# Kernel optimization log

Hardware: AMD Instinct MI355X
Metric: run time of the kernel (lower is better)

The kernel has to match this reference:

```python
import jax, jax.numpy as jnp
import numpy as np

B, S, D, H = 2, 2048, 1024, 16
HD = D // H  # head dim = 64


def setup_inputs() -> dict:
    key = jax.random.key(0)
    ks = jax.random.split(key, 12)
    s = 1.0 / np.sqrt(D)
    return {
        "query": jax.random.normal(ks[0], (B, S, D), jnp.float32),
        "key": jax.random.normal(ks[1], (B, S, D), jnp.float32),
        "value": jax.random.normal(ks[2], (B, S, D), jnp.float32),
        "mask": jax.random.randint(ks[3], (B, S, S), 0, 2, jnp.int32),
        "wq_kernel": jax.random.normal(ks[4], (D, D), jnp.float32) * s,
        "wq_bias": jnp.zeros((D,), jnp.float32),
        "wk_kernel": jax.random.normal(ks[5], (D, D), jnp.float32) * s,
        "wk_bias": jnp.zeros((D,), jnp.float32),
        "wv_kernel": jax.random.normal(ks[6], (D, D), jnp.float32) * s,
        "wv_bias": jnp.zeros((D,), jnp.float32),
        "wo_kernel": jax.random.normal(ks[7], (D, D), jnp.float32) * s,
        "wo_bias": jnp.zeros((D,), jnp.float32),
    }


def reference(query, key, value, mask,
              wq_kernel, wq_bias, wk_kernel, wk_bias,
              wv_kernel, wv_bias, wo_kernel, wo_bias):
    b = query.shape[0]
    # Dense projections, then split heads: [B,S,D] -> [B,H,S,HD]
    def split_heads(x):
        return x.reshape(b, -1, H, HD).transpose(0, 2, 1, 3)

    q = split_heads(query @ wq_kernel + wq_bias)
    k = split_heads(key @ wk_kernel + wk_bias)
    v = split_heads(value @ wv_kernel + wv_bias)

    scores = jnp.einsum('bhqd,bhkd->bhqk', q, k) / jnp.sqrt(jnp.float32(HD))
    m = mask[:, None, :, :]  # [B,1,S,S] broadcast over heads
    scores = jnp.where(m == 0, jnp.float32(-1e9), scores)
    attn = jax.nn.softmax(scores, axis=-1)
    out = jnp.einsum('bhqk,bhkd->bhqd', attn, v)
    out = out.transpose(0, 2, 1, 3).reshape(b, -1, D)  # [B,S,D]
    return out @ wo_kernel + wo_bias
```

## Files before the change

### kernel.cpp

```cpp
#include <hip/hip_runtime.h>
#include <hip/hip_bf16.h>

typedef __attribute__((ext_vector_type(8))) short bf16x8;
typedef __attribute__((ext_vector_type(4))) float f32x4;
typedef __attribute__((ext_vector_type(16))) float f32x16;
typedef __attribute__((ext_vector_type(4))) unsigned int u32x4;
typedef unsigned long long u64;
typedef unsigned short u16;
typedef unsigned int u32;

#define LOG2E 1.44269504088896340736f

__device__ __forceinline__ u16 f2bf(float f) {
  u32 u = __builtin_bit_cast(u32, f);
  u32 r = u + 0x7FFFu + ((u >> 16) & 1u);
  return (u16)(r >> 16);
}

__device__ __forceinline__ u32 cvt_pk_bf16(float lo, float hi) {
  u32 r;
  asm("v_cvt_pk_bf16_f32 %0, %1, %2" : "=v"(r) : "v"(lo), "v"(hi));
  return r;
}

__device__ __forceinline__ void swap32(u32& a, u32& b) {
  asm("v_permlane32_swap_b32 %0, %1" : "+v"(a), "+v"(b));
}

__device__ __forceinline__ float fexp2(float x) {
#if __has_builtin(__builtin_amdgcn_exp2f)
  return __builtin_amdgcn_exp2f(x);
#else
  return exp2f(x);
#endif
}

__device__ __forceinline__ void gload16(const u16* g, u16* l) {
  __builtin_amdgcn_global_load_lds(
      (const __attribute__((address_space(1))) u32*)g,
      (__attribute__((address_space(3))) u32*)l, 16, 0, 0);
}

__global__ __launch_bounds__(256) void mask_bits(const int* __restrict__ mask,
                                                 u64* __restrict__ out) {
  const int nwords = 2 * 2048 * 32;
  int gw = (blockIdx.x * 256 + threadIdx.x) >> 6;
  int lane = threadIdx.x & 63;
  int nw = (gridDim.x * 256) >> 6;
  for (int w = gw; w < nwords; w += nw) {
    int m = mask[(size_t)w * 64 + lane];
    u64 bits = __ballot(m != 0);
    if (lane == 0) out[w] = bits;
  }
}

__global__ __launch_bounds__(256) void wtrans(const float* __restrict__ W0,
                                              const float* __restrict__ W1,
                                              const float* __restrict__ W2,
                                              const float* __restrict__ W3,
                                              u16* __restrict__ WtBase) {
  const float* W = (blockIdx.z == 0) ? W0 : (blockIdx.z == 1) ? W1
                    : (blockIdx.z == 2) ? W2 : W3;
  u16* T = WtBase + (size_t)blockIdx.z * 1048576;
  __shared__ float tile[32][33];
  int k0 = blockIdx.y * 32, n0 = blockIdx.x * 32;
  int tx = threadIdx.x, ty = threadIdx.y;
#pragma unroll
  for (int i = 0; i < 4; i++)
    tile[ty + i * 8][tx] = W[(size_t)(k0 + ty + i * 8) * 1024 + n0 + tx];
  __syncthreads();
#pragma unroll
  for (int i = 0; i < 4; i++)
    T[(size_t)(n0 + ty + i * 8) * 1024 + k0 + tx] = f2bf(tile[tx][ty + i * 8]);
}

__global__ __launch_bounds__(256) void vtrans(const u16* __restrict__ Vb,
                                              u16* __restrict__ Vt) {
  __shared__ u16 t[64][72];
  int bh = blockIdx.y, k0 = blockIdx.x * 64;
  const u16* src = Vb + (size_t)bh * 2048 * 64;
  u16* dst = Vt + (size_t)bh * 64 * 2048;
  int tid = threadIdx.x;
  int r = tid >> 2, c = (tid & 3) * 16;
  *(bf16x8*)&t[r][c] = *(const bf16x8*)(src + (size_t)(k0 + r) * 64 + c);
  *(bf16x8*)&t[r][c + 8] = *(const bf16x8*)(src + (size_t)(k0 + r) * 64 + c + 8);
  __syncthreads();
  int d = tid >> 2, kb = (tid & 3) * 16;
  u16 tmp[16];
#pragma unroll
  for (int i = 0; i < 16; i++) tmp[i] = t[kb + i][d];
  *(bf16x8*)(dst + (size_t)d * 2048 + k0 + kb) = *(bf16x8*)&tmp[0];
  *(bf16x8*)(dst + (size_t)d * 2048 + k0 + kb + 8) = *(bf16x8*)&tmp[8];
}

__global__ __launch_bounds__(256, 2) void gemm_qkv(
    const float* __restrict__ Aq, const float* __restrict__ Ak,
    const float* __restrict__ Av, const float* __restrict__ bq,
    const float* __restrict__ bk, const float* __restrict__ bv,
    const u16* __restrict__ WtBase, u16* __restrict__ OutBase) {
  constexpr int K = 1024;
  __shared__ alignas(16) u16 As[128][40];
  __shared__ alignas(16) u16 Bs[128][32];
  const int fid = blockIdx.x;
  const int c = fid & 7, i = fid >> 3;
  const int panel = c * 12 + (i >> 3);
  const int my = panel & 31, z = panel >> 5;
  const int m0 = my * 128, n0 = (i & 7) * 128;

  const float* A = (z == 0) ? Aq : (z == 1) ? Ak : Av;
  const float* bias = (z == 0) ? bq : (z == 1) ? bk : bv;
  const u16* Bt = WtBase + (size_t)z * 1048576;
  u16* Ob = OutBase + (size_t)z * 4194304;
  const float scale = (z == 0) ? 0.125f * LOG2E : 1.0f;

  const int tid = threadIdx.x;
  const int lane = tid & 63, wave = tid >> 6;
  const int wr = wave >> 1, wc = wave & 1;
  const int fr = lane & 15, fq = lane >> 4;

  const int arow = tid >> 1, ahalf = tid & 1;
  const float* Agp = A + (size_t)(m0 + arow) * K + ahalf * 16;
  const int srow = lane >> 2, scol = (lane & 3) * 8;
  const u16* Bgp = Bt + (size_t)(n0 + wave * 32 + srow) * K + scol;
  u16* Bs0 = &Bs[wave * 32][0];
  u16* Bs1 = &Bs[wave * 32 + 16][0];

  f32x4 acc[4][4];
#pragma unroll
  for (int i2 = 0; i2 < 4; i2++)
#pragma unroll
    for (int j = 0; j < 4; j++) acc[i2][j] = (f32x4){0.f, 0.f, 0.f, 0.f};

  for (int k0 = 0; k0 < K; k0 += 32) {
    float4 a0 = *(const float4*)(Agp + k0);
    float4 a1 = *(const float4*)(Agp + k0 + 4);
    float4 a2 = *(const float4*)(Agp + k0 + 8);
    float4 a3 = *(const float4*)(Agp + k0 + 12);
    gload16(Bgp + k0, Bs0);
    gload16(Bgp + k0 + 16 * K, Bs1);
    __syncthreads();
    u32 c0 = cvt_pk_bf16(a0.x, a0.y), c1 = cvt_pk_bf16(a0.z, a0.w);
    u32 c2 = cvt_pk_bf16(a1.x, a1.y), c3 = cvt_pk_bf16(a1.z, a1.w);
    u32 c4 = cvt_pk_bf16(a2.x, a2.y), c5 = cvt_pk_bf16(a2.z, a2.w);
    u32 c6 = cvt_pk_bf16(a3.x, a3.y), c7 = cvt_pk_bf16(a3.z, a3.w);
    *(u32x4*)&As[arow][ahalf * 16] = (u32x4){c0, c1, c2, c3};
    *(u32x4*)&As[arow][ahalf * 16 + 8] = (u32x4){c4, c5, c6, c7};
    __syncthreads();
    bf16x8 af[4], bfv[4];
#pragma unroll
    for (int i2 = 0; i2 < 4; i2++) {
      af[i2] = *(const bf16x8*)&As[wr * 64 + i2 * 16 + fr][fq * 8];
      bfv[i2] = *(const bf16x8*)&Bs[wc * 64 + i2 * 16 + fr][fq * 8];
    }
#pragma unroll
    for (int i2 = 0; i2 < 4; i2++)
#pragma unroll
      for (int j = 0; j < 4; j++)
        acc[i2][j] = __builtin_amdgcn_mfma_f32_16x16x32_bf16(af[i2], bfv[j],
                                                             acc[i2][j], 0, 0, 0);
  }
#pragma unroll
  for (int j = 0; j < 4; j++) {
    int col = n0 + wc * 64 + j * 16 + fr;
    float bcol = bias[col];
    int hh = col >> 6, hd = col & 63;
#pragma unroll
    for (int i2 = 0; i2 < 4; i2++) {
#pragma unroll
      for (int r = 0; r < 4; r++) {
        int row = m0 + wr * 64 + i2 * 16 + fq * 4 + r;
        int bb = row >> 11, ss = row & 2047;
        float val = (acc[i2][j][r] + bcol) * scale;
        Ob[(((size_t)bb * 16 + hh) * 2048 + ss) * 64 + hd] = f2bf(val);
      }
    }
  }
}

__global__ __launch_bounds__(256, 2) void gemm_out(const u16* __restrict__ A,
                                                   const u16* __restrict__ Bt,
                                                   const float* __restrict__ bias,
                                                   float* __restrict__ Out) {
  constexpr int K = 1024;
  __shared__ alignas(16) u16 As[64][32];
  __shared__ alignas(16) u16 Bs[128][32];
  const int fid = blockIdx.x;
  const int c = fid & 7, i = fid >> 3;
  const int panel = c * 8 + (i >> 3);
  const int m0 = panel * 64, n0 = (i & 7) * 128;

  const int tid = threadIdx.x;
  const int lane = tid & 63, wave = tid >> 6;
  const int wr = wave >> 1, wc = wave & 1;
  const int fr = lane & 15, fq = lane >> 4;

  const int srow = lane >> 2, scol = (lane & 3) * 8;
  const u16* Agp = A + (size_t)(m0 + wave * 16 + srow) * K + scol;
  const u16* Bgp = Bt + (size_t)(n0 + wave * 32 + srow) * K + scol;
  u16* As0 = &As[wave * 16][0];
  u16* Bs0 = &Bs[wave * 32][0];
  u16* Bs1 = &Bs[wave * 32 + 16][0];

  f32x4 acc[2][4];
#pragma unroll
  for (int i2 = 0; i2 < 2; i2++)
#pragma unroll
    for (int j = 0; j < 4; j++) acc[i2][j] = (f32x4){0.f, 0.f, 0.f, 0.f};

  for (int k0 = 0; k0 < K; k0 += 32) {
    gload16(Agp + k0, As0);
    gload16(Bgp + k0, Bs0);
    gload16(Bgp + k0 + 16 * K, Bs1);
    __syncthreads();
    bf16x8 af[2], bfv[4];
#pragma unroll
    for (int i2 = 0; i2 < 2; i2++)
      af[i2] = *(const bf16x8*)&As[wr * 32 + i2 * 16 + fr][fq * 8];
#pragma unroll
    for (int j = 0; j < 4; j++)
      bfv[j] = *(const bf16x8*)&Bs[wc * 64 + j * 16 + fr][fq * 8];
#pragma unroll
    for (int i2 = 0; i2 < 2; i2++)
#pragma unroll
      for (int j = 0; j < 4; j++)
        acc[i2][j] = __builtin_amdgcn_mfma_f32_16x16x32_bf16(af[i2], bfv[j],
                                                             acc[i2][j], 0, 0, 0);
    __syncthreads();
  }
#pragma unroll
  for (int j = 0; j < 4; j++) {
    int col = n0 + wc * 64 + j * 16 + fr;
    float bcol = bias[col];
#pragma unroll
    for (int i2 = 0; i2 < 2; i2++) {
#pragma unroll
      for (int r = 0; r < 4; r++) {
        int row = m0 + wr * 32 + i2 * 16 + fq * 4 + r;
        Out[(size_t)row * 1024 + col] = acc[i2][j][r] + bcol;
      }
    }
  }
}

__global__ __launch_bounds__(512, 4) void attn(const u16* __restrict__ Qb,
                                               const u16* __restrict__ Kb,
                                               const u16* __restrict__ Vtb,
                                               const u64* __restrict__ mbits,
                                               u16* __restrict__ AO) {
  const int fid = blockIdx.x;
  const int nfid = ((fid & 7) << 6) + (fid >> 3);
  const int qt = nfid & 15, bh = nfid >> 4;
  const int h = bh & 15, b = bh >> 4;
  const int q0 = qt * 128;
  const u16* Qh = Qb + (size_t)bh * 2048 * 64;
  const u16* Kh = Kb + (size_t)bh * 2048 * 64;
  const u16* Vh = Vtb + (size_t)bh * 64 * 2048;

  __shared__ alignas(16) u16 smem[32768];
  const int tid = threadIdx.x, lane = tid & 63, wave = tid >> 6;
  const int qw = wave >> 1, kg = wave & 1;
  const int ql = lane & 31, hi = lane >> 5;
  const int l3 = (lane >> 3) & 7, l7 = lane & 7;
  const int srcoff = (l7 ^ l3) * 8;
  const int swz = ql & 7;

  u16* KBg = smem + kg * 8192;
  u16* VBg = smem + 16384 + kg * 8192;
  const int row0 = qw * 16 + l3;

  {
    const u16* ksrc = Kh + (size_t)(kg * 64 + row0) * 64 + srcoff;
    u16* kdst = KBg + (qw * 16) * 64;
    gload16(ksrc, kdst);
    gload16(ksrc + 8 * 64, kdst + 8 * 64);
    const u16* vsrc = Vh + (size_t)row0 * 2048 + kg * 64 + srcoff;
    u16* vdst = VBg + (qw * 16) * 64;
    gload16(vsrc, vdst);
    gload16(vsrc + 8 * 2048, vdst + 8 * 64);
  }
  const int q = q0 + qw * 32 + ql;
  bf16x8 qf[4];
  {
    const u16* qp = Qh + (size_t)q * 64 + hi * 8;
#pragma unroll
    for (int kd = 0; kd < 4; kd++) qf[kd] = *(const bf16x8*)(qp + kd * 16);
  }
  f32x16 accO0, accO1;
#pragma unroll
  for (int i = 0; i < 16; i++) {
    accO0[i] = 0.f;
    accO1[i] = 0.f;
  }
  float lrun = 0.f;
  const u64* mrow = mbits + ((size_t)b * 2048 + q) * 32;
  const u16* kpre = Kh + (size_t)((kg + 2) * 64 + row0) * 64 + srcoff;
  const u16* vpre = Vh + (size_t)row0 * 2048 + (kg + 2) * 64 + srcoff;
  u64 wcur = mrow[kg];
  __syncthreads();

  for (int r = 0; r < 16; r++) {
    const int cur = r & 1;
    const u16* KBc = KBg + cur * 4096;
    const u16* VBc = VBg + cur * 4096;
    u64 wnxt = 0;
    if (r < 15) {
      u16* kdst = KBg + (cur ^ 1) * 4096 + (qw * 16) * 64;
      gload16(kpre, kdst);
      gload16(kpre + 8 * 64, kdst + 8 * 64);
      u16* vdst = VBg + (cur ^ 1) * 4096 + (qw * 16) * 64;
      gload16(vpre, vdst);
      gload16(vpre + 8 * 2048, vdst + 8 * 64);
      kpre += 8192;
      vpre += 128;
      wnxt = mrow[2 * r + kg + 2];
    }
    const u32 wlo = (u32)wcur, wh = (u32)(wcur >> 32);
    bf16x8 pf[4];
    float rs = 0.f;

    {
      f32x16 sf;
#pragma unroll
      for (int g = 0; g < 4; g++) {
        u32 nib = (wlo >> (8 * g + 4 * hi)) & 0xFu;
        sf[4 * g + 0] = (nib & 1u) ? 0.f : -1024.f;
        sf[4 * g + 1] = (nib & 2u) ? 0.f : -1024.f;
        sf[4 * g + 2] = (nib & 4u) ? 0.f : -1024.f;
        sf[4 * g + 3] = (nib & 8u) ? 0.f : -1024.f;
      }
      __builtin_amdgcn_s_setprio(1);
#pragma unroll
      for (int kd = 0; kd < 4; kd++) {
        bf16x8 kf = *(const bf16x8*)&KBc[ql * 64 + ((2 * kd + hi) ^ swz) * 8];
        sf = __builtin_amdgcn_mfma_f32_32x32x16_bf16(kf, qf[kd], sf, 0, 0, 0);
      }
      __builtin_amdgcn_s_setprio(0);
#pragma unroll
      for (int i = 0; i < 16; i++) {
        sf[i] = fexp2(sf[i]);
        rs += sf[i];
      }
      u32 a0 = cvt_pk_bf16(sf[0], sf[1]), a1 = cvt_pk_bf16(sf[2], sf[3]);
      u32 b0 = cvt_pk_bf16(sf[4], sf[5]), b1 = cvt_pk_bf16(sf[6], sf[7]);
      swap32(a0, b0);
      swap32(a1, b1);
      pf[0] = __builtin_bit_cast(bf16x8, (u32x4){a0, a1, b0, b1});
      u32 c0 = cvt_pk_bf16(sf[8], sf[9]), c1 = cvt_pk_bf16(sf[10], sf[11]);
      u32 d0 = cvt_pk_bf16(sf[12], sf[13]), d1 = cvt_pk_bf16(sf[14], sf[15]);
      swap32(c0, d0);
      swap32(c1, d1);
      pf[1] = __builtin_bit_cast(bf16x8, (u32x4){c0, c1, d0, d1});
    }
    {
      f32x16 sf;
#pragma unroll
      for (int g = 0; g < 4; g++) {
        u32 nib = (wh >> (8 * g + 4 * hi)) & 0xFu;
        sf[4 * g + 0] = (nib & 1u) ? 0.f : -1024.f;
        sf[4 * g + 1] = (nib & 2u) ? 0.f : -1024.f;
        sf[4 * g + 2] = (nib & 4u) ? 0.f : -1024.f;
        sf[4 * g + 3] = (nib & 8u) ? 0.f : -1024.f;
      }
      __builtin_amdgcn_s_setprio(1);
#pragma unroll
      for (int kd = 0; kd < 4; kd++) {
        bf16x8 kf =
            *(const bf16x8*)&KBc[(32 + ql) * 64 + ((2 * kd + hi) ^ swz) * 8];
        sf = __builtin_amdgcn_mfma_f32_32x32x16_bf16(kf, qf[kd], sf, 0, 0, 0);
      }
      __builtin_amdgcn_s_setprio(0);
#pragma unroll
      for (int i = 0; i < 16; i++) {
        sf[i] = fexp2(sf[i]);
        rs += sf[i];
      }
      u32 a0 = cvt_pk_bf16(sf[0], sf[1]), a1 = cvt_pk_bf16(sf[2], sf[3]);
      u32 b0 = cvt_pk_bf16(sf[4], sf[5]), b1 = cvt_pk_bf16(sf[6], sf[7]);
      swap32(a0, b0);
      swap32(a1, b1);
      pf[2] = __builtin_bit_cast(bf16x8, (u32x4){a0, a1, b0, b1});
      u32 c0 = cvt_pk_bf16(sf[8], sf[9]), c1 = cvt_pk_bf16(sf[10], sf[11]);
      u32 d0 = cvt_pk_bf16(sf[12], sf[13]), d1 = cvt_pk_bf16(sf[14], sf[15]);
      swap32(c0, d0);
      swap32(c1, d1);
      pf[3] = __builtin_bit_cast(bf16x8, (u32x4){c0, c1, d0, d1});
    }
    rs += __shfl_xor(rs, 32);
    lrun += rs;

    __builtin_amdgcn_s_setprio(1);
#pragma unroll
    for (int ks = 0; ks < 4; ks++) {
      bf16x8 vf0 = *(const bf16x8*)&VBc[ql * 64 + ((2 * ks + hi) ^ swz) * 8];
      bf16x8 vf1 =
          *(const bf16x8*)&VBc[(32 + ql) * 64 + ((2 * ks + hi) ^ swz) * 8];
      accO0 = __builtin_amdgcn_mfma_f32_32x32x16_bf16(vf0, pf[ks], accO0, 0, 0, 0);
      accO1 = __builtin_amdgcn_mfma_f32_32x32x16_bf16(vf1, pf[ks], accO1, 0, 0, 0);
    }
    __builtin_amdgcn_s_setprio(0);
    wcur = wnxt;
    __syncthreads();
  }

  float* MO = (float*)smem;
  float* ML = (float*)((char*)smem + 32768);
  u16* OT = smem + 18432;
  if (kg == 1) {
#pragma unroll
    for (int i = 0; i < 16; i++) {
      int d = (i & 3) + 8 * (i >> 2) + 4 * hi;
      MO[(qw * 64 + d) * 32 + ql] = accO0[i];
      MO[(qw * 64 + 32 + d) * 32 + ql] = accO1[i];
    }
    if (hi == 0) ML[qw * 32 + ql] = lrun;
  }
  __syncthreads();
  if (kg == 0) {
#pragma unroll
    for (int i = 0; i < 16; i++) {
      int d = (i & 3) + 8 * (i >> 2) + 4 * hi;
      accO0[i] += MO[(qw * 64 + d) * 32 + ql];
      accO1[i] += MO[(qw * 64 + 32 + d) * 32 + ql];
    }
    lrun += ML[qw * 32 + ql];
    float inv = 1.f / fmaxf(lrun, 1e-30f);
    const int orow = qw * 32 + ql;
#pragma unroll
    for (int s = 0; s < 8; s++) {
      int d0 = (2 * s & 3) + 8 * (s >> 1) + 4 * hi;
      u32 p0 = cvt_pk_bf16(accO0[2 * s] * inv, accO0[2 * s + 1] * inv);
      u32 p1 = cvt_pk_bf16(accO1[2 * s] * inv, accO1[2 * s + 1] * inv);
      *(u32*)&OT[orow * 72 + d0] = p0;
      *(u32*)&OT[orow * 72 + 32 + d0] = p1;
    }
  }
  __syncthreads();
  {
    int rq = tid >> 2, c0 = (tid & 3) * 16;
    const u16* src = &OT[rq * 72 + c0];
    u16* dst = AO + ((size_t)(b * 2048 + q0 + rq)) * 1024 + h * 64 + c0;
    *(bf16x8*)(dst) = *(const bf16x8*)(src);
    *(bf16x8*)(dst + 8) = *(const bf16x8*)(src + 8);
  }
}

extern "C" void kernel_launch(void* const* d_in, const int* in_sizes, int n_in,
                              void* d_out, int out_size, void* d_ws,
                              size_t ws_size, hipStream_t stream) {
  const float* q = (const float*)d_in[0];
  const float* k = (const float*)d_in[1];
  const float* v = (const float*)d_in[2];
  const int* mask = (const int*)d_in[3];
  const float* wq = (const float*)d_in[4];
  const float* bq = (const float*)d_in[5];
  const float* wk = (const float*)d_in[6];
  const float* bk = (const float*)d_in[7];
  const float* wv = (const float*)d_in[8];
  const float* bv = (const float*)d_in[9];
  const float* wo = (const float*)d_in[10];
  const float* bo = (const float*)d_in[11];

  char* ws = (char*)d_ws;
  u16* Wt = (u16*)(ws);
  u16* Qb = (u16*)(ws + (size_t)(8u << 20));
  u16* Kb = (u16*)(ws + (size_t)(16u << 20));
  u16* Vb = (u16*)(ws + (size_t)(24u << 20));
  u16* AO = (u16*)(ws + (size_t)(32u << 20));
  u64* mb = (u64*)(ws + (size_t)(40u << 20));
  u16* Vt = (u16*)(ws + (size_t)(41u << 20));

  wtrans<<<dim3(32, 32, 4), dim3(32, 8), 0, stream>>>(wq, wk, wv, wo, Wt);
  gemm_qkv<<<dim3(768), dim3(256), 0, stream>>>(q, k, v, bq, bk, bv, Wt, Qb);
  mask_bits<<<dim3(2048), dim3(256), 0, stream>>>(mask, mb);
  vtrans<<<dim3(32, 32), dim3(256), 0, stream>>>(Vb, Vt);
  attn<<<dim3(512), dim3(512), 0, stream>>>(Qb, Kb, Vt, mb, AO);
  gemm_out<<<dim3(512), dim3(256), 0, stream>>>(AO, Wt + 3 * 1048576, bo,
                                                (float*)d_out);
}
```

Baseline: 136.7 us.

## Fuse V transpose into QKV GEMM epilogue, widen K-step, prefetch A, swizzle B

The QKV projection GEMM now writes V straight into transposed [B,H,HD,S] layout in its epilogue, which removes the separate vtrans kernel and its round trip through memory. The main loop moves from a K step of 32 to 64 and register-prefetches the next A tile during the MFMA work. B tiles in LDS use an XOR swizzle to avoid bank conflicts, and occupancy is raised to 3 blocks per CU. The trade-offs are larger LDS use per block, higher register pressure, and the V epilogue writing 8-byte strided stores.

```diff
diff --git a/kernel.cpp b/kernel.cpp
--- a/kernel.cpp
+++ b/kernel.cpp
@@ -74,33 +74,14 @@
     T[(size_t)(n0 + ty + i * 8) * 1024 + k0 + tx] = f2bf(tile[tx][ty + i * 8]);
 }
 
-__global__ __launch_bounds__(256) void vtrans(const u16* __restrict__ Vb,
-                                              u16* __restrict__ Vt) {
-  __shared__ u16 t[64][72];
-  int bh = blockIdx.y, k0 = blockIdx.x * 64;
-  const u16* src = Vb + (size_t)bh * 2048 * 64;
-  u16* dst = Vt + (size_t)bh * 64 * 2048;
-  int tid = threadIdx.x;
-  int r = tid >> 2, c = (tid & 3) * 16;
-  *(bf16x8*)&t[r][c] = *(const bf16x8*)(src + (size_t)(k0 + r) * 64 + c);
-  *(bf16x8*)&t[r][c + 8] = *(const bf16x8*)(src + (size_t)(k0 + r) * 64 + c + 8);
-  __syncthreads();
-  int d = tid >> 2, kb = (tid & 3) * 16;
-  u16 tmp[16];
-#pragma unroll
-  for (int i = 0; i < 16; i++) tmp[i] = t[kb + i][d];
-  *(bf16x8*)(dst + (size_t)d * 2048 + k0 + kb) = *(bf16x8*)&tmp[0];
-  *(bf16x8*)(dst + (size_t)d * 2048 + k0 + kb + 8) = *(bf16x8*)&tmp[8];
-}
-
-__global__ __launch_bounds__(256, 2) void gemm_qkv(
+__global__ __launch_bounds__(256, 3) void gemm_qkv(
     const float* __restrict__ Aq, const float* __restrict__ Ak,
     const float* __restrict__ Av, const float* __restrict__ bq,
     const float* __restrict__ bk, const float* __restrict__ bv,
     const u16* __restrict__ WtBase, u16* __restrict__ OutBase) {
   constexpr int K = 1024;
-  __shared__ alignas(16) u16 As[128][40];
-  __shared__ alignas(16) u16 Bs[128][32];
+  __shared__ alignas(16) u16 As[128][72];
+  __shared__ alignas(16) u16 Bs[128][64];
   const int fid = blockIdx.x;
   const int c = fid & 7, i = fid >> 3;
   const int panel = c * 12 + (i >> 3);
@@ -119,11 +100,11 @@
   const int fr = lane & 15, fq = lane >> 4;
 
   const int arow = tid >> 1, ahalf = tid & 1;
-  const float* Agp = A + (size_t)(m0 + arow) * K + ahalf * 16;
-  const int srow = lane >> 2, scol = (lane & 3) * 8;
-  const u16* Bgp = Bt + (size_t)(n0 + wave * 32 + srow) * K + scol;
-  u16* Bs0 = &Bs[wave * 32][0];
-  u16* Bs1 = &Bs[wave * 32 + 16][0];
+  const float* Agp = A + (size_t)(m0 + arow) * K + ahalf * 32;
+  const int l3 = lane >> 3, l7 = lane & 7;
+  const u16* Bgp = Bt + (size_t)(n0 + wave * 32 + l3) * K + (l7 ^ l3) * 8;
+  u16* Bdst = &Bs[wave * 32][0];
+  const int fsw = fr & 7;
 
   f32x4 acc[4][4];
 #pragma unroll
@@ -131,47 +112,80 @@
 #pragma unroll
     for (int j = 0; j < 4; j++) acc[i2][j] = (f32x4){0.f, 0.f, 0.f, 0.f};
 
-  for (int k0 = 0; k0 < K; k0 += 32) {
-    float4 a0 = *(const float4*)(Agp + k0);
-    float4 a1 = *(const float4*)(Agp + k0 + 4);
-    float4 a2 = *(const float4*)(Agp + k0 + 8);
-    float4 a3 = *(const float4*)(Agp + k0 + 12);
-    gload16(Bgp + k0, Bs0);
-    gload16(Bgp + k0 + 16 * K, Bs1);
+  float4 a[8];
+#pragma unroll
+  for (int t = 0; t < 8; t++) a[t] = *(const float4*)(Agp + t * 4);
+
+  for (int k0 = 0; k0 < K; k0 += 64) {
     __syncthreads();
-    u32 c0 = cvt_pk_bf16(a0.x, a0.y), c1 = cvt_pk_bf16(a0.z, a0.w);
-    u32 c2 = cvt_pk_bf16(a1.x, a1.y), c3 = cvt_pk_bf16(a1.z, a1.w);
-    u32 c4 = cvt_pk_bf16(a2.x, a2.y), c5 = cvt_pk_bf16(a2.z, a2.w);
-    u32 c6 = cvt_pk_bf16(a3.x, a3.y), c7 = cvt_pk_bf16(a3.z, a3.w);
-    *(u32x4*)&As[arow][ahalf * 16] = (u32x4){c0, c1, c2, c3};
-    *(u32x4*)&As[arow][ahalf * 16 + 8] = (u32x4){c4, c5, c6, c7};
+#pragma unroll
+    for (int ch = 0; ch < 4; ch++)
+      gload16(Bgp + k0 + (size_t)ch * 8 * K, Bdst + ch * 512);
+    u32 cc[16];
+#pragma unroll
+    for (int t = 0; t < 8; t++) {
+      cc[2 * t] = cvt_pk_bf16(a[t].x, a[t].y);
+      cc[2 * t + 1] = cvt_pk_bf16(a[t].z, a[t].w);
+    }
+#pragma unroll
+    for (int s = 0; s < 4; s++)
+      *(u32x4*)&As[arow][ahalf * 32 + s * 8] =
+          (u32x4){cc[4 * s], cc[4 * s + 1], cc[4 * s + 2], cc[4 * s + 3]};
     __syncthreads();
-    bf16x8 af[4], bfv[4];
-#pragma unroll
-    for (int i2 = 0; i2 < 4; i2++) {
-      af[i2] = *(const bf16x8*)&As[wr * 64 + i2 * 16 + fr][fq * 8];
-      bfv[i2] = *(const bf16x8*)&Bs[wc * 64 + i2 * 16 + fr][fq * 8];
-    }
-#pragma unroll
-    for (int i2 = 0; i2 < 4; i2++)
-#pragma unroll
-      for (int j = 0; j < 4; j++)
-        acc[i2][j] = __builtin_amdgcn_mfma_f32_16x16x32_bf16(af[i2], bfv[j],
-                                                             acc[i2][j], 0, 0, 0);
-  }
-#pragma unroll
-  for (int j = 0; j < 4; j++) {
-    int col = n0 + wc * 64 + j * 16 + fr;
-    float bcol = bias[col];
-    int hh = col >> 6, hd = col & 63;
-#pragma unroll
-    for (int i2 = 0; i2 < 4; i2++) {
-#pragma unroll
-      for (int r = 0; r < 4; r++) {
-        int row = m0 + wr * 64 + i2 * 16 + fq * 4 + r;
-        int bb = row >> 11, ss = row & 2047;
-        float val = (acc[i2][j][r] + bcol) * scale;
-        Ob[(((size_t)bb * 16 + hh) * 2048 + ss) * 64 + hd] = f2bf(val);
+    if (k0 + 64 < K) {
+#pragma unroll
+      for (int t = 0; t < 8; t++)
+        a[t] = *(const float4*)(Agp + k0 + 64 + t * 4);
+    }
+#pragma unroll
+    for (int kk = 0; kk < 2; kk++) {
+      bf16x8 af[4], bfv[4];
+#pragma unroll
+      for (int i2 = 0; i2 < 4; i2++) {
+        af[i2] = *(const bf16x8*)&As[wr * 64 + i2 * 16 + fr][kk * 32 + fq * 8];
+        bfv[i2] = *(const bf16x8*)
+            &Bs[wc * 64 + i2 * 16 + fr][((kk * 4 + fq) ^ fsw) * 8];
+      }
+#pragma unroll
+      for (int i2 = 0; i2 < 4; i2++)
+#pragma unroll
+        for (int j = 0; j < 4; j++)
+          acc[i2][j] = __builtin_amdgcn_mfma_f32_16x16x32_bf16(
+              af[i2], bfv[j], acc[i2][j], 0, 0, 0);
+    }
+  }
+  if (z == 2) {
+#pragma unroll
+    for (int j = 0; j < 4; j++) {
+      int col = n0 + wc * 64 + j * 16 + fr;
+      float bcol = bias[col];
+      int hh = col >> 6, hd = col & 63;
+#pragma unroll
+      for (int i2 = 0; i2 < 4; i2++) {
+        int row0 = m0 + wr * 64 + i2 * 16 + fq * 4;
+        int bb = row0 >> 11, ss = row0 & 2047;
+        u16 p[4];
+#pragma unroll
+        for (int r = 0; r < 4; r++) p[r] = f2bf(acc[i2][j][r] + bcol);
+        *(u64*)&Ob[((size_t)(bb * 16 + hh) * 64 + hd) * 2048 + ss] =
+            *(u64*)p;
+      }
+    }
+  } else {
+#pragma unroll
+    for (int j = 0; j < 4; j++) {
+      int col = n0 + wc * 64 + j * 16 + fr;
+      float bcol = bias[col];
+      int hh = col >> 6, hd = col & 63;
+#pragma unroll
+      for (int i2 = 0; i2 < 4; i2++) {
+#pragma unroll
+        for (int r = 0; r < 4; r++) {
+          int row = m0 + wr * 64 + i2 * 16 + fq * 4 + r;
+          int bb = row >> 11, ss = row & 2047;
+          float val = (acc[i2][j][r] + bcol) * scale;
+          Ob[(((size_t)bb * 16 + hh) * 2048 + ss) * 64 + hd] = f2bf(val);
+        }
       }
     }
   }
@@ -464,15 +478,13 @@
   u16* Wt = (u16*)(ws);
   u16* Qb = (u16*)(ws + (size_t)(8u << 20));
   u16* Kb = (u16*)(ws + (size_t)(16u << 20));
-  u16* Vb = (u16*)(ws + (size_t)(24u << 20));
+  u16* Vt = (u16*)(ws + (size_t)(24u << 20));
   u16* AO = (u16*)(ws + (size_t)(32u << 20));
   u64* mb = (u64*)(ws + (size_t)(40u << 20));
-  u16* Vt = (u16*)(ws + (size_t)(41u << 20));
 
   wtrans<<<dim3(32, 32, 4), dim3(32, 8), 0, stream>>>(wq, wk, wv, wo, Wt);
   gemm_qkv<<<dim3(768), dim3(256), 0, stream>>>(q, k, v, bq, bk, bv, Wt, Qb);
   mask_bits<<<dim3(2048), dim3(256), 0, stream>>>(mask, mb);
-  vtrans<<<dim3(32, 32), dim3(256), 0, stream>>>(Vb, Vt);
   attn<<<dim3(512), dim3(512), 0, stream>>>(Qb, Kb, Vt, mb, AO);
   gemm_out<<<dim3(512), dim3(256), 0, stream>>>(AO, Wt + 3 * 1048576, bo,
                                                 (float*)d_out);
```

Result: slower. 146.3 us (+7.0%).
